# Kernel optimization log

Measured on AMD Instinct MI355X. Metric: run time of the kernel, lower is better.

## Reference

```python
import math
import jax, jax.numpy as jnp
import numpy as np

D_MODEL = 1024
NUM_HEADS = 16
D_K = D_MODEL // NUM_HEADS
RANK = 16
B, L = 2, 2048


def setup_inputs() -> dict:
    key = jax.random.key(0)
    ks = jax.random.split(key, 10)
    w_scale = 0.02  # keep activations well-scaled like trained linears
    return {
        "x_q": jax.random.normal(ks[0], (B, L, D_MODEL), jnp.float32),
        "x_kv": jax.random.normal(ks[1], (B, L, D_MODEL), jnp.float32),
        "Wq": jax.random.normal(ks[2], (D_MODEL, D_MODEL), jnp.float32) * w_scale,
        "bq": jnp.zeros((D_MODEL,), jnp.float32),
        "Wk": jax.random.normal(ks[3], (D_MODEL, D_MODEL), jnp.float32) * w_scale,
        "bk": jnp.zeros((D_MODEL,), jnp.float32),
        "Wv": jax.random.normal(ks[4], (D_MODEL, D_MODEL), jnp.float32) * w_scale,
        "bv": jnp.zeros((D_MODEL,), jnp.float32),
        "Wo": jax.random.normal(ks[5], (D_MODEL, D_MODEL), jnp.float32) * w_scale,
        "bo": jnp.zeros((D_MODEL,), jnp.float32),
        "U_bil": jax.random.normal(ks[6], (NUM_HEADS, D_K, RANK), jnp.float32) * 0.02,
        "V_bil": jax.random.normal(ks[7], (NUM_HEADS, D_K, RANK), jnp.float32) * 0.02,
        "padding_mask": jnp.zeros((B, L), bool),  # True = padded KV position
    }


def reference(x_q, x_kv, Wq, bq, Wk, bk, Wv, bv, Wo, bo, U_bil, V_bil, padding_mask):
    b, l, _ = x_q.shape
    # torch nn.Linear: y = x @ W.T + b
    Q = (x_q @ Wq.T + bq).reshape(b, l, NUM_HEADS, D_K).transpose(0, 2, 1, 3)  # [B,H,L,dk]
    K = (x_kv @ Wk.T + bk).reshape(b, l, NUM_HEADS, D_K).transpose(0, 2, 1, 3)
    V = (x_kv @ Wv.T + bv).reshape(b, l, NUM_HEADS, D_K).transpose(0, 2, 1, 3)
    # low-rank bilinear projections: [B,H,L,rank]
    Q_proj = jnp.einsum("bhld,hdr->bhlr", Q, U_bil)
    K_proj = jnp.einsum("bhld,hdr->bhlr", K, V_bil)
    scores = jnp.einsum("bhqr,bhkr->bhqk", Q_proj, K_proj) / math.sqrt(RANK)  # [B,H,L,L]
    scores = jnp.where(padding_mask[:, None, None, :], jnp.float32(-10000.0), scores)
    attn = jax.nn.softmax(scores, axis=-1)  # dropout is identity in eval mode
    ctx = jnp.einsum("bhqk,bhkd->bhqd", attn, V)
    ctx = ctx.transpose(0, 2, 1, 3).reshape(b, l, D_MODEL)
    return ctx @ Wo.T + bo
```

## Files before the change

### kernel.cpp

```cpp
#include <hip/hip_runtime.h>
#include <hip/hip_bf16.h>

#define DM   1024
#define NH   16
#define DK   64
#define RK   16
#define BB   2
#define LL   2048
#define TT   (BB*LL)
#define HRK  256


typedef float f4   __attribute__((ext_vector_type(4)));
typedef float f16v __attribute__((ext_vector_type(16)));
typedef short s8v  __attribute__((ext_vector_type(8)));
typedef unsigned int u2v __attribute__((ext_vector_type(2)));
typedef unsigned int u4v __attribute__((ext_vector_type(4)));

static __device__ __forceinline__ unsigned short f2b(float f) {
  __hip_bfloat16 h = __float2bfloat16(f);
  unsigned short u;
  __builtin_memcpy(&u, &h, 2);
  return u;
}
static __device__ __forceinline__ float b2f(unsigned short u) {
  __hip_bfloat16 h;
  __builtin_memcpy(&h, &u, 2);
  return __bfloat162float(h);
}

__global__ __launch_bounds__(256) void cast_all(
    const float* __restrict__ s0, unsigned short* __restrict__ d0, int n0,
    const float* __restrict__ s1, unsigned short* __restrict__ d1, int n1,
    const float* __restrict__ s2, unsigned short* __restrict__ d2, int n2,
    const float* __restrict__ s3, unsigned short* __restrict__ d3, int n3) {
  const float* s; unsigned short* d; int n;
  switch (blockIdx.y) {
    case 0:  s = s0; d = d0; n = n0; break;
    case 1:  s = s1; d = d1; n = n1; break;
    case 2:  s = s2; d = d2; n = n2; break;
    default: s = s3; d = d3; n = n3; break;
  }
  for (int i = blockIdx.x*256 + threadIdx.x; i < n; i += gridDim.x*256) {
    const float4 v = ((const float4*)s)[i];
    ushort4 o;
    o.x = f2b(v.x); o.y = f2b(v.y); o.z = f2b(v.z); o.w = f2b(v.w);
    ((ushort4*)d)[i] = o;
  }
}

__global__ __launch_bounds__(256) void fuse_w(
    const float* __restrict__ Wq, const float* __restrict__ Wk,
    const float* __restrict__ Uq, const float* __restrict__ Uk,
    unsigned short* __restrict__ Aq, unsigned short* __restrict__ Ak) {
  const float* W = blockIdx.z ? Wk : Wq;
  const float* U = blockIdx.z ? Uk : Uq;
  unsigned short* At = blockIdx.z ? Ak : Aq;
  __shared__ float Us[64][16];
  __shared__ float Ws[4][64];
  const int i0 = blockIdx.x * 64;
  const int h  = blockIdx.y;
  const int tid = threadIdx.x;
  const int il = tid & 63, rr = tid >> 6;
  for (int t = tid; t < 64*16; t += 256)
    Us[t >> 4][t & 15] = U[(size_t)(h*DK + (t >> 4))*RK + (t & 15)];
  float acc[4] = {};
  for (int d0 = 0; d0 < DK; d0 += 4) {
    __syncthreads();
    Ws[rr][il] = W[(size_t)(h*DK + d0 + rr)*DM + i0 + il];
    __syncthreads();
#pragma unroll
    for (int dd = 0; dd < 4; ++dd) {
      const float w = Ws[dd][il];
#pragma unroll
      for (int j = 0; j < 4; ++j)
        acc[j] += w * Us[d0 + dd][rr*4 + j];
    }
  }
#pragma unroll
  for (int j = 0; j < 4; ++j)
    At[(size_t)(h*RK + rr*4 + j)*DM + i0 + il] = f2b(acc[j]);
}

__global__ void bias2(const float* __restrict__ bq, const float* __restrict__ bk,
                      const float* __restrict__ Uq, const float* __restrict__ Uk,
                      float* __restrict__ bpq, float* __restrict__ bpk) {
  const int t = threadIdx.x;
  const float* b = (t < 256) ? bq : bk;
  const float* U = (t < 256) ? Uq : Uk;
  float* bp = (t < 256) ? bpq : bpk;
  const int hr = t & 255, h = hr >> 4, r = hr & 15;
  float acc = 0.f;
  for (int d = 0; d < DK; ++d)
    acc += b[h*DK + d] * U[(size_t)(h*DK + d)*RK + r];
  bp[hr] = acc;
}

__global__ __launch_bounds__(256) void vsum_k(
    const unsigned short* __restrict__ Vt, float* __restrict__ Vsum) {
  const int h = blockIdx.x, b = blockIdx.y;
  const int d = threadIdx.x >> 2, part = threadIdx.x & 3;
  const unsigned short* row = Vt + ((size_t)b*DM + h*DK + d)*LL + part*512;
  float s = 0.f;
  for (int i = 0; i < 512; i += 8) {
    const s8v v = *(const s8v*)&row[i];
#pragma unroll
    for (int j = 0; j < 8; ++j) s += b2f((unsigned short)v[j]);
  }
  s += __shfl_xor(s, 1);
  s += __shfl_xor(s, 2);
  if (part == 0) Vsum[((size_t)b*NH + h)*DK + d] = s;
}

template<int N_, int MODE, int AF32>
__global__ __launch_bounds__(256) void gemm64(
    const void* __restrict__ A0, const void* __restrict__ A1,
    const unsigned short* __restrict__ B0, const unsigned short* __restrict__ B1,
    const float* __restrict__ bi0, const float* __restrict__ bi1,
    void* __restrict__ C0, void* __restrict__ C1) {
  const void* Agv = blockIdx.z ? A1 : A0;
  const unsigned short* Bg = blockIdx.z ? B1 : B0;
  const float* bias = blockIdx.z ? bi1 : bi0;
  void* Cgv = blockIdx.z ? C1 : C0;
  __shared__ unsigned short Xs[64*40];
  __shared__ unsigned short Bs[128*40];
  const int t0 = blockIdx.x * 64, n0 = blockIdx.y * 128;
  const int tid = threadIdx.x, wave = tid >> 6, lane = tid & 63;
  const int quad = lane >> 4, l15 = lane & 15;
  const int nh = wave * 32;

  const f4 z = {0.f, 0.f, 0.f, 0.f};
  f4 acc[4][2];
#pragma unroll
  for (int a = 0; a < 4; ++a) { acc[a][0] = z; acc[a][1] = z; }

  for (int k0 = 0; k0 < DM; k0 += 32) {
    __syncthreads();
    {
      const int ar = tid >> 2, ap = tid & 3;
      if (AF32) {
        const float* Af = (const float*)Agv;
        const float4 x0 = *(const float4*)&Af[(size_t)(t0 + ar)*DM + k0 + ap*8];
        const float4 x1 = *(const float4*)&Af[(size_t)(t0 + ar)*DM + k0 + ap*8 + 4];
        s8v v;
        v[0]=(short)f2b(x0.x); v[1]=(short)f2b(x0.y);
        v[2]=(short)f2b(x0.z); v[3]=(short)f2b(x0.w);
        v[4]=(short)f2b(x1.x); v[5]=(short)f2b(x1.y);
        v[6]=(short)f2b(x1.z); v[7]=(short)f2b(x1.w);
        *(s8v*)&Xs[ar*40 + ap*8] = v;
      } else {
        *(s8v*)&Xs[ar*40 + ap*8] =
            *(const s8v*)&((const unsigned short*)Agv)[(size_t)(t0 + ar)*DM + k0 + ap*8];
      }
      const int br = tid >> 1, bp = tid & 1;
      *(s8v*)&Bs[br*40 + bp*16] =
          *(const s8v*)&Bg[(size_t)(n0 + br)*DM + k0 + bp*16];
      *(s8v*)&Bs[br*40 + bp*16 + 8] =
          *(const s8v*)&Bg[(size_t)(n0 + br)*DM + k0 + bp*16 + 8];
    }
    __syncthreads();

    s8v af[4], bf[2];
#pragma unroll
    for (int ms = 0; ms < 4; ++ms)
      af[ms] = *(const s8v*)&Xs[(ms*16 + l15)*40 + quad*8];
#pragma unroll
    for (int ns = 0; ns < 2; ++ns)
      bf[ns] = *(const s8v*)&Bs[(nh + ns*16 + l15)*40 + quad*8];
#pragma unroll
    for (int ms = 0; ms < 4; ++ms)
#pragma unroll
      for (int ns = 0; ns < 2; ++ns)
        acc[ms][ns] = __builtin_amdgcn_mfma_f32_16x16x32_bf16(
            af[ms], bf[ns], acc[ms][ns], 0, 0, 0);
  }

#pragma unroll
  for (int ms = 0; ms < 4; ++ms) {
    const int tb = t0 + ms*16 + quad*4;
#pragma unroll
    for (int ns = 0; ns < 2; ++ns) {
      const int o = n0 + nh + ns*16 + l15;
      const float bv = bias[o];
      f4 a = acc[ms][ns];
      if (MODE == 0) {
        float* C = (float*)Cgv;
#pragma unroll
        for (int rg = 0; rg < 4; ++rg)
          C[(size_t)(tb + rg)*N_ + o] = a[rg] + bv;
      } else if (MODE == 1) {
        unsigned short* C = (unsigned short*)Cgv;
#pragma unroll
        for (int rg = 0; rg < 4; ++rg)
          C[(size_t)(tb + rg)*N_ + o] = f2b(a[rg] + bv);
      } else {
        unsigned short* C = (unsigned short*)Cgv;
        const int bb = tb >> 11, l = tb & 2047;
        ushort4 pk;
        pk.x = f2b(a[0] + bv); pk.y = f2b(a[1] + bv);
        pk.z = f2b(a[2] + bv); pk.w = f2b(a[3] + bv);
        *(ushort4*)&C[((size_t)bb*DM + o)*LL + l] = pk;
      }
    }
  }
}

template<bool MASKED>
static __device__ __forceinline__ void softmax_pack(
    const f16v& s0, const f16v& s1, const unsigned long long mb, const int hi,
    float& den, unsigned int (&Pd)[2][4][2]) {
#pragma unroll
  for (int nt = 0; nt < 2; ++nt) {
    const f16v& sv = nt ? s1 : s0;
#pragma unroll
    for (int r = 0; r < 4; ++r) {
      float ep[4];
#pragma unroll
      for (int j = 0; j < 4; ++j) {
        float em = __expf(sv[r*4 + j] * 0.25f);
        if (MASKED) {
          const int kloc = nt*32 + j + 8*r + 4*hi;
          if ((mb >> kloc) & 1ull) em = 0.f;
        }
        den += em;
        ep[j] = em - 1.f;
      }
      asm("v_cvt_pk_bf16_f32 %0, %1, %2"
          : "=v"(Pd[nt][r][0]) : "v"(ep[0]), "v"(ep[1]));
      asm("v_cvt_pk_bf16_f32 %0, %1, %2"
          : "=v"(Pd[nt][r][1]) : "v"(ep[2]), "v"(ep[3]));
    }
  }
}

__global__ __launch_bounds__(256) void attention_v5(
    const unsigned short* __restrict__ Qp, const unsigned short* __restrict__ Kp,
    const unsigned short* __restrict__ Vt, const float* __restrict__ Vsum,
    const unsigned char* __restrict__ msk, float* __restrict__ ctx) {
  __shared__ __align__(16) unsigned short Ks[2][2][64][8];
  __shared__ __align__(16) unsigned short Vs[2][8][64][8];
  __shared__ float denW[4][32];
  const int q0 = blockIdx.x * 128, h = blockIdx.y, b = blockIdx.z;
  const int tid = threadIdx.x, w = tid >> 6, lane = tid & 63;
  const int l31 = lane & 31, hi = lane >> 5;

  const s8v qfrag = *(const s8v*)&Qp[
      (size_t)(b*LL + q0 + w*32 + l31)*HRK + h*RK + hi*8];

  const int sr = tid >> 2, sp = tid & 3;
  const unsigned short* __restrict__ Vrow =
      Vt + ((size_t)b*DM + h*DK + sr)*LL;
  const unsigned short* __restrict__ Kbase =
      Kp + ((size_t)b*LL + sr)*HRK + h*RK + sp*4;
  const unsigned char*  __restrict__ Mrow = msk + (size_t)b*LL + lane;

  u2v kpre; s8v vpre0, vpre1;
  unsigned char mcur, mnext;

  kpre  = *(const u2v*)&Kbase[0];
  vpre0 = *(const s8v*)&Vrow[sp*16];
  vpre1 = *(const s8v*)&Vrow[sp*16 + 8];
  mcur  = Mrow[0];
  *(u2v*)&Ks[0][sp>>1][sr][(sp&1)*4] = kpre;
  *(s8v*)&Vs[0][sp*2][sr][0]   = vpre0;
  *(s8v*)&Vs[0][sp*2+1][sr][0] = vpre1;
  kpre  = *(const u2v*)&Kbase[(size_t)64*HRK];
  vpre0 = *(const s8v*)&Vrow[64 + sp*16];
  vpre1 = *(const s8v*)&Vrow[64 + sp*16 + 8];
  mnext = Mrow[64];
  __syncthreads();

  f16v acc0, acc1, z16;
#pragma unroll
  for (int i = 0; i < 16; ++i) { acc0[i] = 0.f; acc1[i] = 0.f; z16[i] = 0.f; }
  float den = 0.f;

  for (int t = 0; t < LL/64; ++t) {
    const int cur = t & 1;
    const unsigned long long mb = __ballot(mcur != 0);

    const s8v kf0 = *(const s8v*)&Ks[cur][hi][l31][0];
    const s8v kf1 = *(const s8v*)&Ks[cur][hi][32 + l31][0];
    s8v vf[4][2];
#pragma unroll
    for (int kc = 0; kc < 4; ++kc) {
      vf[kc][0] = *(const s8v*)&Vs[cur][kc*2 + hi][l31][0];
      vf[kc][1] = *(const s8v*)&Vs[cur][kc*2 + hi][32 + l31][0];
    }

    const f16v s0 = __builtin_amdgcn_mfma_f32_32x32x16_bf16(kf0, qfrag, z16, 0, 0, 0);
    const f16v s1 = __builtin_amdgcn_mfma_f32_32x32x16_bf16(kf1, qfrag, z16, 0, 0, 0);

    unsigned int Pd[2][4][2];
    if (__builtin_expect(mb != 0ull, 0))
      softmax_pack<true >(s0, s1, mb, hi, den, Pd);
    else
      softmax_pack<false>(s0, s1, mb, hi, den, Pd);

#pragma unroll
    for (int kc = 0; kc < 4; ++kc) {
      const int nt = kc >> 1, a = (kc & 1)*2;
      const unsigned int p00 = Pd[nt][a][0],   p01 = Pd[nt][a][1];
      const unsigned int p10 = Pd[nt][a+1][0], p11 = Pd[nt][a+1][1];
      const unsigned int e0 = __shfl_xor(hi ? p00 : p10, 32);
      const unsigned int e1 = __shfl_xor(hi ? p01 : p11, 32);
      u4v efi;
      efi[0] = hi ? e0 : p00;
      efi[1] = hi ? e1 : p01;
      efi[2] = hi ? p10 : e0;
      efi[3] = hi ? p11 : e1;
      const s8v ef = __builtin_bit_cast(s8v, efi);
      acc0 = __builtin_amdgcn_mfma_f32_32x32x16_bf16(ef, vf[kc][0], acc0, 0, 0, 0);
      acc1 = __builtin_amdgcn_mfma_f32_32x32x16_bf16(ef, vf[kc][1], acc1, 0, 0, 0);
    }

    if (t + 1 < LL/64) {
      *(u2v*)&Ks[cur^1][sp>>1][sr][(sp&1)*4] = kpre;
      *(s8v*)&Vs[cur^1][sp*2][sr][0]   = vpre0;
      *(s8v*)&Vs[cur^1][sp*2+1][sr][0] = vpre1;
      const int tn = (t + 2 < LL/64) ? t + 2 : LL/64 - 1;
      kpre  = *(const u2v*)&Kbase[(size_t)tn*64*HRK];
      vpre0 = *(const s8v*)&Vrow[tn*64 + sp*16];
      vpre1 = *(const s8v*)&Vrow[tn*64 + sp*16 + 8];
      mcur  = mnext;
      mnext = Mrow[tn*64];
    }
    __syncthreads();
  }

  den += __shfl_xor(den, 32);
  if (hi == 0) denW[w][l31] = 1.f / fmaxf(den, 1e-30f);

  const float vs0 = Vsum[((size_t)b*NH + h)*DK + l31];
  const float vs1 = Vsum[((size_t)b*NH + h)*DK + 32 + l31];

#pragma unroll
  for (int rg = 0; rg < 16; ++rg) {
    const int qr = (rg & 3) + 8*(rg >> 2) + 4*hi;
    const float inv = denW[w][qr];
    const size_t row = (size_t)(b*LL + q0 + w*32 + qr)*DM + h*DK;
    ctx[row + l31]      = (vs0 + acc0[rg]) * inv;
    ctx[row + 32 + l31] = (vs1 + acc1[rg]) * inv;
  }
}

extern "C" void kernel_launch(void* const* d_in, const int* in_sizes, int n_in,
                              void* d_out, int out_size, void* d_ws, size_t ws_size,
                              hipStream_t stream) {
  (void)in_sizes; (void)n_in; (void)out_size; (void)ws_size;
  const float* x_q   = (const float*)d_in[0];
  const float* x_kv  = (const float*)d_in[1];
  const float* Wq    = (const float*)d_in[2];
  const float* bq    = (const float*)d_in[3];
  const float* Wk    = (const float*)d_in[4];
  const float* bk    = (const float*)d_in[5];
  const float* Wv    = (const float*)d_in[6];
  const float* bv    = (const float*)d_in[7];
  const float* Wo    = (const float*)d_in[8];
  const float* bo    = (const float*)d_in[9];
  const float* U_bil = (const float*)d_in[10];
  const float* V_bil = (const float*)d_in[11];
  const unsigned char* pmask = (const unsigned char*)d_in[12];
  float* out = (float*)d_out;

  char* w = (char*)d_ws;
  unsigned short* xq_b  = (unsigned short*)(w);
  unsigned short* xkv_b = (unsigned short*)(w +  8388608);
  unsigned short* Wv_b  = (unsigned short*)(w + 16777216);
  unsigned short* Wo_b  = (unsigned short*)(w + 18874368);
  unsigned short* Atq   = (unsigned short*)(w + 20971520);
  unsigned short* Atk   = (unsigned short*)(w + 21495808);
  float*          bpq   = (float*)(w + 22020096);
  float*          bpk   = (float*)(w + 22021120);
  unsigned short* Qp    = (unsigned short*)(w + 22022144);
  unsigned short* Kp    = (unsigned short*)(w + 24119296);
  unsigned short* Vt    = (unsigned short*)(w + 26216448);
  float*          Vsum  = (float*)(w + 34605056);
  float*          ctx   = (float*)w;

  cast_all<<<dim3(1024, 4), 256, 0, stream>>>(
      x_q, xq_b, TT*DM/4, x_kv, xkv_b, TT*DM/4,
      Wv, Wv_b, DM*DM/4,  Wo, Wo_b, DM*DM/4);
  fuse_w<<<dim3(DM/64, NH, 2), 256, 0, stream>>>(Wq, Wk, U_bil, V_bil, Atq, Atk);
  bias2<<<1, 512, 0, stream>>>(bq, bk, U_bil, V_bil, bpq, bpk);
  gemm64<HRK, 1, 0><<<dim3(64, 2, 2), 256, 0, stream>>>(
      xq_b, xkv_b, Atq, Atk, bpq, bpk, Qp, Kp);
  gemm64<DM, 2, 0><<<dim3(64, 8, 1), 256, 0, stream>>>(
      xkv_b, xkv_b, Wv_b, Wv_b, bv, bv, Vt, Vt);
  vsum_k<<<dim3(NH, BB), 256, 0, stream>>>(Vt, Vsum);
  attention_v5<<<dim3(LL/128, NH, BB), 256, 0, stream>>>(
      Qp, Kp, Vt, Vsum, pmask, ctx);
  gemm64<DM, 0, 1><<<dim3(64, 8, 1), 256, 0, stream>>>(
      ctx, ctx, Wo_b, Wo_b, bo, bo, out, out);
}
```

Baseline: 276.7 us.

## Load attention K/V fragments directly from global memory and drop LDS staging

The attention kernel no longer stages K and V tiles through shared memory with double buffering and block barriers. Each wave instead loads its MFMA fragments straight from global memory into registers, one tile ahead. The Q/K projection GEMM now writes a head-major [B,H,L,16] layout so each fragment is a contiguous 16-byte load. The denominator broadcast uses a warp shuffle instead of shared memory. This removes LDS traffic and __syncthreads, but the four waves in a block now each fetch the same K/V data redundantly and rely on cache, and register pressure goes up.

```diff
diff --git a/kernel.cpp b/kernel.cpp
--- a/kernel.cpp
+++ b/kernel.cpp
@@ -14,7 +14,6 @@
 typedef float f4   __attribute__((ext_vector_type(4)));
 typedef float f16v __attribute__((ext_vector_type(16)));
 typedef short s8v  __attribute__((ext_vector_type(8)));
-typedef unsigned int u2v __attribute__((ext_vector_type(2)));
 typedef unsigned int u4v __attribute__((ext_vector_type(4)));
 
 static __device__ __forceinline__ unsigned short f2b(float f) {
@@ -191,8 +190,11 @@
       } else if (MODE == 1) {
         unsigned short* C = (unsigned short*)Cgv;
 #pragma unroll
-        for (int rg = 0; rg < 4; ++rg)
-          C[(size_t)(tb + rg)*N_ + o] = f2b(a[rg] + bv);
+        for (int rg = 0; rg < 4; ++rg) {
+          const int tt = tb + rg;
+          C[(((size_t)(tt >> 11)*NH + (o >> 4))*LL + (tt & 2047))*RK + (o & 15)]
+              = f2b(a[rg] + bv);
+        }
       } else {
         unsigned short* C = (unsigned short*)Cgv;
         const int bb = tb >> 11, l = tb & 2047;
@@ -233,63 +235,58 @@
   }
 }
 
-__global__ __launch_bounds__(256) void attention_v5(
+__global__ __launch_bounds__(256) void attention_v6(
     const unsigned short* __restrict__ Qp, const unsigned short* __restrict__ Kp,
     const unsigned short* __restrict__ Vt, const float* __restrict__ Vsum,
     const unsigned char* __restrict__ msk, float* __restrict__ ctx) {
-  __shared__ __align__(16) unsigned short Ks[2][2][64][8];
-  __shared__ __align__(16) unsigned short Vs[2][8][64][8];
-  __shared__ float denW[4][32];
   const int q0 = blockIdx.x * 128, h = blockIdx.y, b = blockIdx.z;
   const int tid = threadIdx.x, w = tid >> 6, lane = tid & 63;
   const int l31 = lane & 31, hi = lane >> 5;
 
   const s8v qfrag = *(const s8v*)&Qp[
-      (size_t)(b*LL + q0 + w*32 + l31)*HRK + h*RK + hi*8];
-
-  const int sr = tid >> 2, sp = tid & 3;
-  const unsigned short* __restrict__ Vrow =
-      Vt + ((size_t)b*DM + h*DK + sr)*LL;
-  const unsigned short* __restrict__ Kbase =
-      Kp + ((size_t)b*LL + sr)*HRK + h*RK + sp*4;
+      (((size_t)b*NH + h)*LL + q0 + w*32 + l31)*RK + hi*8];
+
+  const unsigned short* __restrict__ Kl =
+      Kp + (((size_t)b*NH + h)*LL + l31)*RK + hi*8;
+  const unsigned short* __restrict__ Vl0 =
+      Vt + ((size_t)b*DM + h*DK + l31)*LL + hi*8;
+  const unsigned short* __restrict__ Vl1 = Vl0 + (size_t)32*LL;
   const unsigned char*  __restrict__ Mrow = msk + (size_t)b*LL + lane;
 
-  u2v kpre; s8v vpre0, vpre1;
-  unsigned char mcur, mnext;
-
-  kpre  = *(const u2v*)&Kbase[0];
-  vpre0 = *(const s8v*)&Vrow[sp*16];
-  vpre1 = *(const s8v*)&Vrow[sp*16 + 8];
-  mcur  = Mrow[0];
-  *(u2v*)&Ks[0][sp>>1][sr][(sp&1)*4] = kpre;
-  *(s8v*)&Vs[0][sp*2][sr][0]   = vpre0;
-  *(s8v*)&Vs[0][sp*2+1][sr][0] = vpre1;
-  kpre  = *(const u2v*)&Kbase[(size_t)64*HRK];
-  vpre0 = *(const s8v*)&Vrow[64 + sp*16];
-  vpre1 = *(const s8v*)&Vrow[64 + sp*16 + 8];
-  mnext = Mrow[64];
-  __syncthreads();
+  s8v kc0 = *(const s8v*)&Kl[0];
+  s8v kc1 = *(const s8v*)&Kl[32*RK];
+  s8v vc[4][2];
+#pragma unroll
+  for (int kc = 0; kc < 4; ++kc) {
+    vc[kc][0] = *(const s8v*)&Vl0[kc*16];
+    vc[kc][1] = *(const s8v*)&Vl1[kc*16];
+  }
+  unsigned char mcur = Mrow[0];
 
   f16v acc0, acc1, z16;
 #pragma unroll
   for (int i = 0; i < 16; ++i) { acc0[i] = 0.f; acc1[i] = 0.f; z16[i] = 0.f; }
   float den = 0.f;
 
+#pragma unroll 2
   for (int t = 0; t < LL/64; ++t) {
-    const int cur = t & 1;
+    const int tn = (t + 1 < LL/64) ? t + 1 : t;
+    const size_t ko = (size_t)tn*64*RK;
+    const int    vo = tn*64;
+    const s8v kn0 = *(const s8v*)&Kl[ko];
+    const s8v kn1 = *(const s8v*)&Kl[ko + 32*RK];
+    s8v vn[4][2];
+#pragma unroll
+    for (int kc = 0; kc < 4; ++kc) {
+      vn[kc][0] = *(const s8v*)&Vl0[vo + kc*16];
+      vn[kc][1] = *(const s8v*)&Vl1[vo + kc*16];
+    }
+    const unsigned char mnext = Mrow[vo];
+
     const unsigned long long mb = __ballot(mcur != 0);
 
-    const s8v kf0 = *(const s8v*)&Ks[cur][hi][l31][0];
-    const s8v kf1 = *(const s8v*)&Ks[cur][hi][32 + l31][0];
-    s8v vf[4][2];
-#pragma unroll
-    for (int kc = 0; kc < 4; ++kc) {
-      vf[kc][0] = *(const s8v*)&Vs[cur][kc*2 + hi][l31][0];
-      vf[kc][1] = *(const s8v*)&Vs[cur][kc*2 + hi][32 + l31][0];
-    }
-
-    const f16v s0 = __builtin_amdgcn_mfma_f32_32x32x16_bf16(kf0, qfrag, z16, 0, 0, 0);
-    const f16v s1 = __builtin_amdgcn_mfma_f32_32x32x16_bf16(kf1, qfrag, z16, 0, 0, 0);
+    const f16v s0 = __builtin_amdgcn_mfma_f32_32x32x16_bf16(kc0, qfrag, z16, 0, 0, 0);
+    const f16v s1 = __builtin_amdgcn_mfma_f32_32x32x16_bf16(kc1, qfrag, z16, 0, 0, 0);
 
     unsigned int Pd[2][4][2];
     if (__builtin_expect(mb != 0ull, 0))
@@ -310,26 +307,21 @@
       efi[2] = hi ? p10 : e0;
       efi[3] = hi ? p11 : e1;
       const s8v ef = __builtin_bit_cast(s8v, efi);
-      acc0 = __builtin_amdgcn_mfma_f32_32x32x16_bf16(ef, vf[kc][0], acc0, 0, 0, 0);
-      acc1 = __builtin_amdgcn_mfma_f32_32x32x16_bf16(ef, vf[kc][1], acc1, 0, 0, 0);
-    }
-
-    if (t + 1 < LL/64) {
-      *(u2v*)&Ks[cur^1][sp>>1][sr][(sp&1)*4] = kpre;
-      *(s8v*)&Vs[cur^1][sp*2][sr][0]   = vpre0;
-      *(s8v*)&Vs[cur^1][sp*2+1][sr][0] = vpre1;
-      const int tn = (t + 2 < LL/64) ? t + 2 : LL/64 - 1;
-      kpre  = *(const u2v*)&Kbase[(size_t)tn*64*HRK];
-      vpre0 = *(const s8v*)&Vrow[tn*64 + sp*16];
-      vpre1 = *(const s8v*)&Vrow[tn*64 + sp*16 + 8];
-      mcur  = mnext;
-      mnext = Mrow[tn*64];
-    }
-    __syncthreads();
+      acc0 = __builtin_amdgcn_mfma_f32_32x32x16_bf16(ef, vc[kc][0], acc0, 0, 0, 0);
+      acc1 = __builtin_amdgcn_mfma_f32_32x32x16_bf16(ef, vc[kc][1], acc1, 0, 0, 0);
+    }
+
+    kc0 = kn0; kc1 = kn1;
+#pragma unroll
+    for (int kc = 0; kc < 4; ++kc) {
+      vc[kc][0] = vn[kc][0];
+      vc[kc][1] = vn[kc][1];
+    }
+    mcur = mnext;
   }
 
   den += __shfl_xor(den, 32);
-  if (hi == 0) denW[w][l31] = 1.f / fmaxf(den, 1e-30f);
+  const float inv = 1.f / fmaxf(den, 1e-30f);
 
   const float vs0 = Vsum[((size_t)b*NH + h)*DK + l31];
   const float vs1 = Vsum[((size_t)b*NH + h)*DK + 32 + l31];
@@ -337,10 +329,10 @@
 #pragma unroll
   for (int rg = 0; rg < 16; ++rg) {
     const int qr = (rg & 3) + 8*(rg >> 2) + 4*hi;
-    const float inv = denW[w][qr];
+    const float invq = __shfl(inv, qr);
     const size_t row = (size_t)(b*LL + q0 + w*32 + qr)*DM + h*DK;
-    ctx[row + l31]      = (vs0 + acc0[rg]) * inv;
-    ctx[row + 32 + l31] = (vs1 + acc1[rg]) * inv;
+    ctx[row + l31]      = (vs0 + acc0[rg]) * invq;
+    ctx[row + 32 + l31] = (vs1 + acc1[rg]) * invq;
   }
 }
 
@@ -388,7 +380,7 @@
   gemm64<DM, 2, 0><<<dim3(64, 8, 1), 256, 0, stream>>>(
       xkv_b, xkv_b, Wv_b, Wv_b, bv, bv, Vt, Vt);
   vsum_k<<<dim3(NH, BB), 256, 0, stream>>>(Vt, Vsum);
-  attention_v5<<<dim3(LL/128, NH, BB), 256, 0, stream>>>(
+  attention_v6<<<dim3(LL/128, NH, BB), 256, 0, stream>>>(
       Qp, Kp, Vt, Vsum, pmask, ctx);
   gemm64<DM, 0, 1><<<dim3(64, 8, 1), 256, 0, stream>>>(
       ctx, ctx, Wo_b, Wo_b, bo, bo, out, out);
```

New measurement: 297.6 us. 1.08x slower.

## Split attention over KV halves with separate reduce kernel and head-major Q/K layout

Applied to the files above, without the earlier changes.

Splits the KV sequence into two halves so the attention grid doubles from 512 to 1024 blocks. Each split writes unnormalized bf16 partial contexts and per-row denominators, and a new reduce kernel combines them, adds Vsum and normalizes in place into the ctx buffer. The projected Q/K are also stored head-major so K tiles are contiguous, and V fragment loads move into the PV loop to lower register pressure. The cost is an extra kernel launch, extra global traffic for the partials, and bf16 rounding of the partial accumulators.

```diff
diff --git a/kernel.cpp b/kernel.cpp
--- a/kernel.cpp
+++ b/kernel.cpp
@@ -9,6 +9,7 @@
 #define LL   2048
 #define TT   (BB*LL)
 #define HRK  256
+#define NSPL 2
 
 
 typedef float f4   __attribute__((ext_vector_type(4)));
@@ -191,8 +192,11 @@
       } else if (MODE == 1) {
         unsigned short* C = (unsigned short*)Cgv;
 #pragma unroll
-        for (int rg = 0; rg < 4; ++rg)
-          C[(size_t)(tb + rg)*N_ + o] = f2b(a[rg] + bv);
+        for (int rg = 0; rg < 4; ++rg) {
+          const int tt = tb + rg;
+          C[(((size_t)(tt >> 11)*NH + (o >> 4))*LL + (tt & 2047))*RK + (o & 15)]
+              = f2b(a[rg] + bv);
+        }
       } else {
         unsigned short* C = (unsigned short*)Cgv;
         const int bb = tb >> 11, l = tb & 2047;
@@ -233,26 +237,29 @@
   }
 }
 
-__global__ __launch_bounds__(256) void attention_v5(
+__global__ __launch_bounds__(256) void attention_v7(
     const unsigned short* __restrict__ Qp, const unsigned short* __restrict__ Kp,
-    const unsigned short* __restrict__ Vt, const float* __restrict__ Vsum,
-    const unsigned char* __restrict__ msk, float* __restrict__ ctx) {
+    const unsigned short* __restrict__ Vt,
+    const unsigned char* __restrict__ msk,
+    unsigned short* __restrict__ P, float* __restrict__ denP) {
   __shared__ __align__(16) unsigned short Ks[2][2][64][8];
   __shared__ __align__(16) unsigned short Vs[2][8][64][8];
-  __shared__ float denW[4][32];
-  const int q0 = blockIdx.x * 128, h = blockIdx.y, b = blockIdx.z;
+  const int q0 = blockIdx.x * 128, h = blockIdx.y;
+  const int b = blockIdx.z & (BB - 1), ksp = blockIdx.z >> 1;
+  const int kbeg = ksp * (LL / NSPL);
+  const int NT = (LL / NSPL) / 64;
   const int tid = threadIdx.x, w = tid >> 6, lane = tid & 63;
   const int l31 = lane & 31, hi = lane >> 5;
 
   const s8v qfrag = *(const s8v*)&Qp[
-      (size_t)(b*LL + q0 + w*32 + l31)*HRK + h*RK + hi*8];
+      (((size_t)b*NH + h)*LL + q0 + w*32 + l31)*RK + hi*8];
 
   const int sr = tid >> 2, sp = tid & 3;
   const unsigned short* __restrict__ Vrow =
-      Vt + ((size_t)b*DM + h*DK + sr)*LL;
+      Vt + ((size_t)b*DM + h*DK + sr)*LL + kbeg;
   const unsigned short* __restrict__ Kbase =
-      Kp + ((size_t)b*LL + sr)*HRK + h*RK + sp*4;
-  const unsigned char*  __restrict__ Mrow = msk + (size_t)b*LL + lane;
+      Kp + (((size_t)b*NH + h)*LL + kbeg + sr)*RK + sp*4;
+  const unsigned char*  __restrict__ Mrow = msk + (size_t)b*LL + kbeg + lane;
 
   u2v kpre; s8v vpre0, vpre1;
   unsigned char mcur, mnext;
@@ -264,7 +271,7 @@
   *(u2v*)&Ks[0][sp>>1][sr][(sp&1)*4] = kpre;
   *(s8v*)&Vs[0][sp*2][sr][0]   = vpre0;
   *(s8v*)&Vs[0][sp*2+1][sr][0] = vpre1;
-  kpre  = *(const u2v*)&Kbase[(size_t)64*HRK];
+  kpre  = *(const u2v*)&Kbase[(size_t)64*RK];
   vpre0 = *(const s8v*)&Vrow[64 + sp*16];
   vpre1 = *(const s8v*)&Vrow[64 + sp*16 + 8];
   mnext = Mrow[64];
@@ -275,18 +282,12 @@
   for (int i = 0; i < 16; ++i) { acc0[i] = 0.f; acc1[i] = 0.f; z16[i] = 0.f; }
   float den = 0.f;
 
-  for (int t = 0; t < LL/64; ++t) {
+  for (int t = 0; t < NT; ++t) {
     const int cur = t & 1;
     const unsigned long long mb = __ballot(mcur != 0);
 
     const s8v kf0 = *(const s8v*)&Ks[cur][hi][l31][0];
     const s8v kf1 = *(const s8v*)&Ks[cur][hi][32 + l31][0];
-    s8v vf[4][2];
-#pragma unroll
-    for (int kc = 0; kc < 4; ++kc) {
-      vf[kc][0] = *(const s8v*)&Vs[cur][kc*2 + hi][l31][0];
-      vf[kc][1] = *(const s8v*)&Vs[cur][kc*2 + hi][32 + l31][0];
-    }
 
     const f16v s0 = __builtin_amdgcn_mfma_f32_32x32x16_bf16(kf0, qfrag, z16, 0, 0, 0);
     const f16v s1 = __builtin_amdgcn_mfma_f32_32x32x16_bf16(kf1, qfrag, z16, 0, 0, 0);
@@ -310,16 +311,18 @@
       efi[2] = hi ? p10 : e0;
       efi[3] = hi ? p11 : e1;
       const s8v ef = __builtin_bit_cast(s8v, efi);
-      acc0 = __builtin_amdgcn_mfma_f32_32x32x16_bf16(ef, vf[kc][0], acc0, 0, 0, 0);
-      acc1 = __builtin_amdgcn_mfma_f32_32x32x16_bf16(ef, vf[kc][1], acc1, 0, 0, 0);
-    }
-
-    if (t + 1 < LL/64) {
+      const s8v vf0 = *(const s8v*)&Vs[cur][kc*2 + hi][l31][0];
+      const s8v vf1 = *(const s8v*)&Vs[cur][kc*2 + hi][32 + l31][0];
+      acc0 = __builtin_amdgcn_mfma_f32_32x32x16_bf16(ef, vf0, acc0, 0, 0, 0);
+      acc1 = __builtin_amdgcn_mfma_f32_32x32x16_bf16(ef, vf1, acc1, 0, 0, 0);
+    }
+
+    if (t + 1 < NT) {
       *(u2v*)&Ks[cur^1][sp>>1][sr][(sp&1)*4] = kpre;
       *(s8v*)&Vs[cur^1][sp*2][sr][0]   = vpre0;
       *(s8v*)&Vs[cur^1][sp*2+1][sr][0] = vpre1;
-      const int tn = (t + 2 < LL/64) ? t + 2 : LL/64 - 1;
-      kpre  = *(const u2v*)&Kbase[(size_t)tn*64*HRK];
+      const int tn = (t + 2 < NT) ? t + 2 : NT - 1;
+      kpre  = *(const u2v*)&Kbase[(size_t)tn*64*RK];
       vpre0 = *(const s8v*)&Vrow[tn*64 + sp*16];
       vpre1 = *(const s8v*)&Vrow[tn*64 + sp*16 + 8];
       mcur  = mnext;
@@ -329,19 +332,38 @@
   }
 
   den += __shfl_xor(den, 32);
-  if (hi == 0) denW[w][l31] = 1.f / fmaxf(den, 1e-30f);
-
-  const float vs0 = Vsum[((size_t)b*NH + h)*DK + l31];
-  const float vs1 = Vsum[((size_t)b*NH + h)*DK + 32 + l31];
+  if (hi == 0)
+    denP[(((size_t)ksp*BB + b)*NH + h)*LL + q0 + w*32 + l31] = den;
 
 #pragma unroll
   for (int rg = 0; rg < 16; ++rg) {
     const int qr = (rg & 3) + 8*(rg >> 2) + 4*hi;
-    const float inv = denW[w][qr];
-    const size_t row = (size_t)(b*LL + q0 + w*32 + qr)*DM + h*DK;
-    ctx[row + l31]      = (vs0 + acc0[rg]) * inv;
-    ctx[row + 32 + l31] = (vs1 + acc1[rg]) * inv;
-  }
+    const size_t base = 2*(((size_t)(b*LL + q0 + w*32 + qr))*DM + h*DK) + ksp;
+    P[base + 2*l31]        = f2b(acc0[rg]);
+    P[base + 2*(32 + l31)] = f2b(acc1[rg]);
+  }
+}
+
+__global__ __launch_bounds__(256) void reduce_k(
+    unsigned int* __restrict__ P, const float* __restrict__ Vsum,
+    const float* __restrict__ denP) {
+  const size_t j0 = ((size_t)blockIdx.x*256 + threadIdx.x)*4;
+  const int t  = (int)(j0 >> 10);
+  const int dm = (int)(j0 & 1023);
+  const int b = t >> 11, l = t & 2047;
+  const int h = dm >> 6, d = dm & 63;
+  const float dn =
+      denP[((size_t)b*NH + h)*LL + l] +
+      denP[(((size_t)BB + b)*NH + h)*LL + l];
+  const float inv = 1.f / fmaxf(dn, 1e-30f);
+  const f4 vs = *(const f4*)&Vsum[((size_t)b*NH + h)*DK + d];
+  const u4v p = *(const u4v*)&P[j0];
+  f4 c;
+#pragma unroll
+  for (int i = 0; i < 4; ++i)
+    c[i] = (vs[i] + b2f((unsigned short)(p[i] & 0xffff))
+                  + b2f((unsigned short)(p[i] >> 16))) * inv;
+  *(f4*)&P[j0] = c;
 }
 
 extern "C" void kernel_launch(void* const* d_in, const int* in_sizes, int n_in,
@@ -376,6 +398,8 @@
   unsigned short* Kp    = (unsigned short*)(w + 24119296);
   unsigned short* Vt    = (unsigned short*)(w + 26216448);
   float*          Vsum  = (float*)(w + 34605056);
+  float*          denP  = (float*)(w + 34613248);
+  unsigned short* Pbuf  = (unsigned short*)w;
   float*          ctx   = (float*)w;
 
   cast_all<<<dim3(1024, 4), 256, 0, stream>>>(
@@ -388,8 +412,9 @@
   gemm64<DM, 2, 0><<<dim3(64, 8, 1), 256, 0, stream>>>(
       xkv_b, xkv_b, Wv_b, Wv_b, bv, bv, Vt, Vt);
   vsum_k<<<dim3(NH, BB), 256, 0, stream>>>(Vt, Vsum);
-  attention_v5<<<dim3(LL/128, NH, BB), 256, 0, stream>>>(
-      Qp, Kp, Vt, Vsum, pmask, ctx);
+  attention_v7<<<dim3(LL/128, NH, BB*NSPL), 256, 0, stream>>>(
+      Qp, Kp, Vt, pmask, Pbuf, denP);
+  reduce_k<<<dim3(TT*DM/1024), 256, 0, stream>>>((unsigned int*)w, Vsum, denP);
   gemm64<DM, 0, 1><<<dim3(64, 8, 1), 256, 0, stream>>>(
       ctx, ctx, Wo_b, Wo_b, bo, bo, out, out);
 }
```

New measurement: 265.5 us. 4.1% less time.
